# Performance work log

Measured on AMD Instinct MI355X. Metric: run time of the kernel, lower is better.

The kernel has to match this reference:

```python
import jax, jax.numpy as jnp
import numpy as np

DIM = 512
CTX_DIM = 512
NUM_HEADS = 8
DIM_HEAD = 64
INNER = NUM_HEADS * DIM_HEAD  # 512
B, N, CTX_LEN = 4, 2048, 2048


def setup_inputs() -> dict:
    key = jax.random.key(0)
    ks = jax.random.split(key, 6)
    x = jax.random.normal(ks[0], (B, DIM, N), dtype=jnp.float32)
    context = jax.random.normal(ks[1], (B, CTX_DIM, CTX_LEN), dtype=jnp.float32)
    # Linear weights stored as (in, out); bias only on output projection.
    W_q = jax.random.normal(ks[2], (DIM, INNER), dtype=jnp.float32) / np.sqrt(DIM)
    W_kv = jax.random.normal(ks[3], (CTX_DIM, 2 * INNER), dtype=jnp.float32) / np.sqrt(CTX_DIM)
    W_out = jax.random.normal(ks[4], (INNER, DIM), dtype=jnp.float32) / np.sqrt(INNER)
    b_out = jax.random.normal(ks[5], (DIM,), dtype=jnp.float32) * 0.01
    return {"x": x, "context": context, "W_q": W_q, "W_kv": W_kv,
            "W_out": W_out, "b_out": b_out}


def reference(x, context, W_q, W_kv, W_out, b_out):
    scale = DIM_HEAD ** -0.5
    xs = jnp.swapaxes(x, 1, 2)        # (b, n, dim)
    cs = jnp.swapaxes(context, 1, 2)  # (b, ctx_len, ctx_dim)
    b, n, _ = xs.shape
    m = cs.shape[1]
    q = xs @ W_q                       # (b, n, inner)
    kv = cs @ W_kv                     # (b, m, 2*inner)
    k, v = jnp.split(kv, 2, axis=-1)
    # split heads -> (b, h, len, d)
    q = q.reshape(b, n, NUM_HEADS, DIM_HEAD).transpose(0, 2, 1, 3)
    k = k.reshape(b, m, NUM_HEADS, DIM_HEAD).transpose(0, 2, 1, 3)
    v = v.reshape(b, m, NUM_HEADS, DIM_HEAD).transpose(0, 2, 1, 3)
    attn = jnp.einsum('bhqd,bhkd->bhqk', q * scale, k)
    attn = jax.nn.softmax(attn, axis=-1)
    out = jnp.einsum('bhqk,bhkd->bhqd', attn, v)
    out = out.transpose(0, 2, 1, 3).reshape(b, n, INNER)
    out = out @ W_out + b_out          # (b, n, dim); dropout p=0 is identity
    return jnp.swapaxes(out, 1, 2)     # (b, dim, n)
```

## Files before the change

kernel.cpp:

```cpp
#include <hip/hip_runtime.h>
#include <hip/hip_bf16.h>

typedef __attribute__((ext_vector_type(8))) short bf16x8;
typedef __attribute__((ext_vector_type(4))) float f32x4;
typedef __attribute__((ext_vector_type(16))) float f32x16;
typedef __attribute__((ext_vector_type(8))) unsigned short ushort8v;
typedef __attribute__((ext_vector_type(4))) unsigned short ushort4v;

#define MFMA16(a, b, c) __builtin_amdgcn_mfma_f32_16x16x32_bf16((a), (b), (c), 0, 0, 0)
#define MFMA32(a, b, c) __builtin_amdgcn_mfma_f32_32x32x16_bf16((a), (b), (c), 0, 0, 0)

__device__ __forceinline__ unsigned short f2bf(float f) {
  union { float f; unsigned int u; } v; v.f = f;
  unsigned int r = v.u + 0x7FFFu + ((v.u >> 16) & 1u);
  return (unsigned short)(r >> 16);
}

__device__ __forceinline__ unsigned int cvtpk(float a, float b) {
  unsigned int r;
  asm("v_cvt_pk_bf16_f32 %0, %1, %2" : "=v"(r) : "v"(a), "v"(b));
  return r;
}

__global__ __launch_bounds__(256) void transpose_all_kernel(
    const float* __restrict__ x, const float* __restrict__ ctx,
    const float* __restrict__ Wq, const float* __restrict__ Wkv,
    const float* __restrict__ Wo, unsigned short* __restrict__ xt,
    unsigned short* __restrict__ ct, unsigned short* __restrict__ Wqt,
    unsigned short* __restrict__ Wkvt, unsigned short* __restrict__ Wot) {
  __shared__ float tile[64][33];
  int z = blockIdx.z;
  const float* in;
  unsigned short* out;
  int C;
  if (z < 4)      { in = x + (size_t)z * 512 * 2048;         out = xt + (size_t)z * 2048 * 512;        C = 2048; }
  else if (z < 8) { in = ctx + (size_t)(z - 4) * 512 * 2048; out = ct + (size_t)(z - 4) * 2048 * 512;  C = 2048; }
  else if (z == 8) { in = Wq;  out = Wqt;  C = 512; }
  else if (z == 9) { in = Wkv; out = Wkvt; C = 1024; }
  else             { in = Wo;  out = Wot;  C = 512; }
  int c0 = blockIdx.x * 32;
  if (c0 >= C) return;
  int r0 = blockIdx.y * 64;
  int tid = threadIdx.x, cl = tid & 31, rl = tid >> 5;
#pragma unroll
  for (int k = 0; k < 8; ++k)
    tile[rl + 8 * k][cl] = in[(size_t)(r0 + rl + 8 * k) * C + c0 + cl];
  __syncthreads();
  int c = tid >> 3, rc = (tid & 7) * 8;
  ushort8v p;
#pragma unroll
  for (int jj = 0; jj < 8; ++jj) p[jj] = f2bf(tile[rc + jj][c]);
  *(ushort8v*)&out[(size_t)(c0 + c) * 512 + r0 + rc] = p;
}

__device__ __forceinline__ void gemm_acc128(
    const unsigned short* __restrict__ A, const unsigned short* __restrict__ Bt,
    int l0, int o0, f32x4 acc[4][4],
    unsigned short (*As)[80], unsigned short (*Bs)[80]) {
  int tid = threadIdx.x, lane = tid & 63, wave = tid >> 6;
  int wl = wave >> 1, wo = wave & 1, lg = lane >> 4, lr = lane & 15;
  for (int kb = 0; kb < 512; kb += 64) {
    {
      int row = tid >> 1, cc = (tid & 1) * 32;
      const ushort8v* srca = (const ushort8v*)(A + (size_t)(l0 + row) * 512 + kb + cc);
      const ushort8v* srcb = (const ushort8v*)(Bt + (size_t)(o0 + row) * 512 + kb + cc);
#pragma unroll
      for (int i = 0; i < 4; ++i) *(ushort8v*)&As[row][cc + 8 * i] = srca[i];
#pragma unroll
      for (int i = 0; i < 4; ++i) *(ushort8v*)&Bs[row][cc + 8 * i] = srcb[i];
    }
    __syncthreads();
#pragma unroll
    for (int kc = 0; kc < 2; ++kc) {
      bf16x8 af[4], bfr[4];
#pragma unroll
      for (int mf = 0; mf < 4; ++mf)
        af[mf] = *(const bf16x8*)&As[wl * 64 + mf * 16 + lr][kc * 32 + 8 * lg];
#pragma unroll
      for (int nf = 0; nf < 4; ++nf)
        bfr[nf] = *(const bf16x8*)&Bs[wo * 64 + nf * 16 + lr][kc * 32 + 8 * lg];
#pragma unroll
      for (int mf = 0; mf < 4; ++mf)
#pragma unroll
        for (int nf = 0; nf < 4; ++nf)
          acc[mf][nf] = MFMA16(af[mf], bfr[nf], acc[mf][nf]);
    }
    __syncthreads();
  }
}

__global__ __launch_bounds__(256) void gemm_qkv_kernel(
    const unsigned short* __restrict__ xt, const unsigned short* __restrict__ ct,
    const unsigned short* __restrict__ Wqt, const unsigned short* __restrict__ Wkvt,
    unsigned short* __restrict__ Qb, unsigned short* __restrict__ K,
    unsigned short* __restrict__ Vt) {
  __shared__ unsigned short As[128][80];
  __shared__ unsigned short Bs[128][80];
  f32x4 acc[4][4] = {};
  int l0 = blockIdx.x * 128;
  int yy = blockIdx.y;
  const unsigned short* A;
  const unsigned short* Bt;
  int o0;
  if (yy < 4) { A = xt; Bt = Wqt; o0 = yy * 128; }
  else        { A = ct; Bt = Wkvt; o0 = (yy - 4) * 128; }
  gemm_acc128(A, Bt, l0, o0, acc, As, Bs);
  int lane = threadIdx.x & 63, wave = threadIdx.x >> 6;
  int wl = wave >> 1, wo = wave & 1, lg = lane >> 4, lr = lane & 15;
  if (yy < 4) {
    const float qs = 0.18033688011112042f;
#pragma unroll
    for (int mf = 0; mf < 4; ++mf)
#pragma unroll
      for (int nf = 0; nf < 4; ++nf)
#pragma unroll
        for (int r = 0; r < 4; ++r) {
          int row = l0 + wl * 64 + mf * 16 + 4 * lg + r;
          int col = o0 + wo * 64 + nf * 16 + lr;
          Qb[(size_t)row * 512 + col] = f2bf(acc[mf][nf][r] * qs);
        }
  } else if (o0 < 512) {
#pragma unroll
    for (int mf = 0; mf < 4; ++mf)
#pragma unroll
      for (int nf = 0; nf < 4; ++nf)
#pragma unroll
        for (int r = 0; r < 4; ++r) {
          int row = l0 + wl * 64 + mf * 16 + 4 * lg + r;
          int col = o0 + wo * 64 + nf * 16 + lr;
          K[(size_t)row * 512 + col] = f2bf(acc[mf][nf][r]);
        }
  } else {
    int b = l0 >> 11;
#pragma unroll
    for (int mf = 0; mf < 4; ++mf)
#pragma unroll
      for (int nf = 0; nf < 4; ++nf) {
        int m0v = (l0 & 2047) + wl * 64 + mf * 16 + 4 * lg;
        int msw = (m0v & ~12) | ((m0v & 4) << 1) | ((m0v & 8) >> 1);
        int oh = (o0 - 512) + wo * 64 + nf * 16 + lr;
        int h = oh >> 6, d = oh & 63;
        ushort4v pk;
#pragma unroll
        for (int r = 0; r < 4; ++r) pk[r] = f2bf(acc[mf][nf][r]);
        *(ushort4v*)&Vt[(size_t)((b * 8 + h) * 64 + d) * 2048 + msw] = pk;
      }
  }
}

__global__ __launch_bounds__(256) void gemm_out_kernel(
    const unsigned short* __restrict__ A, const unsigned short* __restrict__ Bt,
    float* __restrict__ Out, const float* __restrict__ bias) {
  __shared__ unsigned short As[128][80];
  __shared__ unsigned short Bs[128][80];
  f32x4 acc[4][4] = {};
  int l0 = blockIdx.x * 128, o0 = blockIdx.y * 128;
  gemm_acc128(A, Bt, l0, o0, acc, As, Bs);
  int lane = threadIdx.x & 63, wave = threadIdx.x >> 6;
  int wl = wave >> 1, wo = wave & 1, lg = lane >> 4, lr = lane & 15;
#pragma unroll
  for (int mf = 0; mf < 4; ++mf)
#pragma unroll
    for (int nf = 0; nf < 4; ++nf) {
      int row = l0 + wl * 64 + mf * 16 + 4 * lg;
      int col = o0 + wo * 64 + nf * 16 + lr;
      int b = row >> 11, n = row & 2047;
      float bv = bias[col];
      f32x4 v = acc[mf][nf];
#pragma unroll
      for (int r = 0; r < 4; ++r) v[r] += bv;
      *(f32x4*)&Out[((size_t)(b * 512 + col)) * 2048 + n] = v;
    }
}

__global__ __launch_bounds__(128, 2) void attn_kernel(
    const unsigned short* __restrict__ Qb, const unsigned short* __restrict__ Kb,
    const unsigned short* __restrict__ Vt, unsigned short* __restrict__ Ob) {
  __shared__ unsigned short Ksh[2][4160];
  __shared__ unsigned short Vsh[2][4160];
  int id = blockIdx.x;
  int slot = id & 7, qb = (id >> 3) & 31, hbhi = id >> 8;
  int hb = hbhi * 8 + slot;
  int h = hb & 7, b = hb >> 3;
  int tid = threadIdx.x, w = tid >> 6, lane = tid & 63;
  int l31 = lane & 31, hi = lane >> 5;
  int qrow = b * 2048 + qb * 64 + w * 32 + l31;

  const unsigned short* qp = Qb + (size_t)qrow * 512 + h * 64 + 8 * hi;
  bf16x8 qf[4];
#pragma unroll
  for (int dk = 0; dk < 4; ++dk) qf[dk] = *(const bf16x8*)(qp + 16 * dk);

  int r8 = lane >> 3, gc = (lane & 7) ^ r8;
  const unsigned short* kg =
      Kb + (size_t)(b * 2048 + w * 32 + r8) * 512 + h * 64 + gc * 8;
  const unsigned short* vg =
      Vt + (size_t)((b * 8 + h) * 64 + w * 32 + r8) * 2048 + gc * 8;
  int grp0 = w * 4;

#define STAGE(t, bi)                                                               \
  {                                                                                \
    _Pragma("unroll") for (int j2 = 0; j2 < 4; ++j2) {                             \
      __builtin_amdgcn_global_load_lds(                                            \
          (const __attribute__((address_space(1))) void*)(kg +                     \
              (size_t)((t) * 64 + j2 * 8) * 512),                                  \
          (__attribute__((address_space(3))) void*)(&Ksh[bi][(grp0 + j2) * 520]),  \
          16, 0, 0);                                                               \
      __builtin_amdgcn_global_load_lds(                                            \
          (const __attribute__((address_space(1))) void*)(vg +                     \
              (size_t)(j2 * 8) * 2048 + (t) * 64),                                 \
          (__attribute__((address_space(3))) void*)(&Vsh[bi][(grp0 + j2) * 520]),  \
          16, 0, 0);                                                               \
    }                                                                              \
  }

  STAGE(0, 0);
  STAGE(1, 1);

  int rowoff0 = (l31 >> 3) * 1040 + (l31 & 7) * 128;
  int rowoff1 = rowoff0 + 4 * 1040;
  int swz = (l31 & 7) << 4;

  f32x16 o0 = {}, o1 = {};
  float lsum = 0.0f;

#pragma unroll 1
  for (int t = 0; t < 32; ++t) {
    int bi = t & 1;
    if (t == 31) { asm volatile("s_waitcnt vmcnt(0)" ::: "memory"); }
    else         { asm volatile("s_waitcnt vmcnt(8)" ::: "memory"); }
    __builtin_amdgcn_sched_barrier(0);
    __builtin_amdgcn_s_barrier();
    __builtin_amdgcn_sched_barrier(0);

    const char* kbC = (const char*)&Ksh[bi][0];
    const char* vbC = (const char*)&Vsh[bi][0];
    bf16x8 kfr[8];
#pragma unroll
    for (int dk = 0; dk < 4; ++dk) {
      kfr[dk] = *(const bf16x8*)(kbC + rowoff0 + (((2 * dk + hi) << 4) ^ swz));
      kfr[4 + dk] = *(const bf16x8*)(kbC + rowoff1 + (((2 * dk + hi) << 4) ^ swz));
    }
    bf16x8 vfa[4], vfb[4];
#pragma unroll
    for (int q = 0; q < 4; ++q) {
      vfa[q] = *(const bf16x8*)(vbC + rowoff0 + (((2 * q + hi) << 4) ^ swz));
      vfb[q] = *(const bf16x8*)(vbC + rowoff1 + (((2 * q + hi) << 4) ^ swz));
    }
    asm volatile("s_waitcnt lgkmcnt(0)" ::: "memory");
    __builtin_amdgcn_sched_barrier(0);
    __builtin_amdgcn_s_barrier();
    __builtin_amdgcn_sched_barrier(0);
    if (t < 30) STAGE(t + 2, bi);

    __builtin_amdgcn_s_setprio(1);
    f32x16 sA = {}, sB = {};
#pragma unroll
    for (int dk = 0; dk < 4; ++dk) {
      sA = MFMA32(kfr[dk], qf[dk], sA);
      sB = MFMA32(kfr[4 + dk], qf[dk], sB);
    }
    __builtin_amdgcn_s_setprio(0);

#pragma unroll
    for (int i = 0; i < 16; ++i) {
      sA[i] = __builtin_amdgcn_exp2f(sA[i]);
      sB[i] = __builtin_amdgcn_exp2f(sB[i]);
    }
    float u[8];
#pragma unroll
    for (int i = 0; i < 8; ++i) u[i] = (sA[i] + sA[i + 8]) + (sB[i] + sB[i + 8]);
    lsum += ((u[0] + u[1]) + (u[2] + u[3])) + ((u[4] + u[5]) + (u[6] + u[7]));

    bf16x8 ptA[2], ptB[2];
    {
      union { unsigned int wd[4]; bf16x8 v; } uu;
      uu.wd[0] = cvtpk(sA[0], sA[1]); uu.wd[1] = cvtpk(sA[2], sA[3]);
      uu.wd[2] = cvtpk(sA[4], sA[5]); uu.wd[3] = cvtpk(sA[6], sA[7]);
      ptA[0] = uu.v;
      uu.wd[0] = cvtpk(sA[8], sA[9]); uu.wd[1] = cvtpk(sA[10], sA[11]);
      uu.wd[2] = cvtpk(sA[12], sA[13]); uu.wd[3] = cvtpk(sA[14], sA[15]);
      ptA[1] = uu.v;
      uu.wd[0] = cvtpk(sB[0], sB[1]); uu.wd[1] = cvtpk(sB[2], sB[3]);
      uu.wd[2] = cvtpk(sB[4], sB[5]); uu.wd[3] = cvtpk(sB[6], sB[7]);
      ptB[0] = uu.v;
      uu.wd[0] = cvtpk(sB[8], sB[9]); uu.wd[1] = cvtpk(sB[10], sB[11]);
      uu.wd[2] = cvtpk(sB[12], sB[13]); uu.wd[3] = cvtpk(sB[14], sB[15]);
      ptB[1] = uu.v;
    }

    __builtin_amdgcn_s_setprio(1);
    o0 = MFMA32(vfa[0], ptA[0], o0);
    o0 = MFMA32(vfa[1], ptA[1], o0);
    o1 = MFMA32(vfb[0], ptA[0], o1);
    o1 = MFMA32(vfb[1], ptA[1], o1);
    o0 = MFMA32(vfa[2], ptB[0], o0);
    o0 = MFMA32(vfa[3], ptB[1], o0);
    o1 = MFMA32(vfb[2], ptB[0], o1);
    o1 = MFMA32(vfb[3], ptB[1], o1);
    __builtin_amdgcn_s_setprio(0);
  }
#undef STAGE

  float ltot = lsum + __shfl_xor(lsum, 32, 64);
  float rinv = 1.0f / ltot;
  unsigned short* ob = Ob + (size_t)qrow * 512 + h * 64 + 4 * hi;
#pragma unroll
  for (int i = 0; i < 8; ++i) {
    int dvlo = ((2 * i) & 3) + 8 * ((2 * i) >> 2);
    *(unsigned int*)(ob + dvlo) = cvtpk(o0[2 * i] * rinv, o0[2 * i + 1] * rinv);
    *(unsigned int*)(ob + 32 + dvlo) = cvtpk(o1[2 * i] * rinv, o1[2 * i + 1] * rinv);
  }
}

extern "C" void kernel_launch(void* const* d_in, const int* in_sizes, int n_in,
                              void* d_out, int out_size, void* d_ws, size_t ws_size,
                              hipStream_t stream) {
  const float* x   = (const float*)d_in[0];
  const float* ctx = (const float*)d_in[1];
  const float* Wq  = (const float*)d_in[2];
  const float* Wkv = (const float*)d_in[3];
  const float* Wo  = (const float*)d_in[4];
  const float* bo  = (const float*)d_in[5];
  float* out = (float*)d_out;

  char* ws = (char*)d_ws;
  unsigned short* xt   = (unsigned short*)(ws + 0);
  unsigned short* ct   = (unsigned short*)(ws + 8388608);
  unsigned short* Wqt  = (unsigned short*)(ws + 16777216);
  unsigned short* Wkvt = (unsigned short*)(ws + 17301504);
  unsigned short* Wot  = (unsigned short*)(ws + 18350080);
  unsigned short* Qb   = (unsigned short*)(ws + 18874368);
  unsigned short* Kb   = (unsigned short*)(ws + 27262976);
  unsigned short* Vtb  = (unsigned short*)(ws + 35651584);
  unsigned short* Ob   = (unsigned short*)(ws + 44040192);

  transpose_all_kernel<<<dim3(64, 8, 11), 256, 0, stream>>>(
      x, ctx, Wq, Wkv, Wo, xt, ct, Wqt, Wkvt, Wot);

  gemm_qkv_kernel<<<dim3(64, 12), 256, 0, stream>>>(xt, ct, Wqt, Wkvt, Qb, Kb, Vtb);

  attn_kernel<<<dim3(1024), 128, 0, stream>>>(Qb, Kb, Vtb, Ob);

  gemm_out_kernel<<<dim3(64, 4), 256, 0, stream>>>(Ob, Wot, out, bo);
}
```

Measured before the change: 110.9 us.

## Use direct global-to-LDS loads with XOR-swizzled layout in projection GEMMs

Replaces the register-staged global-to-shared copies in the shared GEMM tile routine with global_load_lds direct-to-LDS transfers. The shared-memory layout becomes an XOR-swizzled 8-row block layout so MFMA fragment reads avoid bank conflicts. Separately, bf16 conversion switches from manual integer rounding to the packed hardware v_cvt_pk_bf16_f32 instruction in the transpose and epilogues. This removes VGPR staging and conversion ALU work, at the cost of more complex addressing. The main attention kernel is unaffected, so the overall effect is bounded by the GEMM share of the total time.

```diff
diff --git a/kernel.cpp b/kernel.cpp
--- a/kernel.cpp
+++ b/kernel.cpp
@@ -10,16 +10,13 @@
 #define MFMA16(a, b, c) __builtin_amdgcn_mfma_f32_16x16x32_bf16((a), (b), (c), 0, 0, 0)
 #define MFMA32(a, b, c) __builtin_amdgcn_mfma_f32_32x32x16_bf16((a), (b), (c), 0, 0, 0)
 
-__device__ __forceinline__ unsigned short f2bf(float f) {
-  union { float f; unsigned int u; } v; v.f = f;
-  unsigned int r = v.u + 0x7FFFu + ((v.u >> 16) & 1u);
-  return (unsigned short)(r >> 16);
-}
-
 __device__ __forceinline__ unsigned int cvtpk(float a, float b) {
   unsigned int r;
   asm("v_cvt_pk_bf16_f32 %0, %1, %2" : "=v"(r) : "v"(a), "v"(b));
   return r;
+}
+__device__ __forceinline__ unsigned short f2bf(float f) {
+  return (unsigned short)cvtpk(f, f);
 }
 
 __global__ __launch_bounds__(256) void transpose_all_kernel(
@@ -47,27 +44,43 @@
     tile[rl + 8 * k][cl] = in[(size_t)(r0 + rl + 8 * k) * C + c0 + cl];
   __syncthreads();
   int c = tid >> 3, rc = (tid & 7) * 8;
-  ushort8v p;
-#pragma unroll
-  for (int jj = 0; jj < 8; ++jj) p[jj] = f2bf(tile[rc + jj][c]);
-  *(ushort8v*)&out[(size_t)(c0 + c) * 512 + r0 + rc] = p;
+  union { unsigned int wd[4]; ushort8v v; } p;
+#pragma unroll
+  for (int jj = 0; jj < 4; ++jj)
+    p.wd[jj] = cvtpk(tile[rc + 2 * jj][c], tile[rc + 2 * jj + 1][c]);
+  *(ushort8v*)&out[(size_t)(c0 + c) * 512 + r0 + rc] = p.v;
 }
 
 __device__ __forceinline__ void gemm_acc128(
     const unsigned short* __restrict__ A, const unsigned short* __restrict__ Bt,
     int l0, int o0, f32x4 acc[4][4],
-    unsigned short (*As)[80], unsigned short (*Bs)[80]) {
-  int tid = threadIdx.x, lane = tid & 63, wave = tid >> 6;
-  int wl = wave >> 1, wo = wave & 1, lg = lane >> 4, lr = lane & 15;
+    unsigned short* As, unsigned short* Bs) {
+  int tid = threadIdx.x, lane = tid & 63, wv = tid >> 6;
+  int wl = wv >> 1, wo = wv & 1, lg = lane >> 4, lr = lane & 15;
+  int r8 = lane >> 3, gc = (lane & 7) ^ r8;
+  const unsigned short* ga = A + (size_t)(l0 + wv * 32 + r8) * 512 + gc * 8;
+  const unsigned short* gb = Bt + (size_t)(o0 + wv * 32 + r8) * 512 + gc * 8;
+  int rowbA[4], rswA[4], rowbB[4], rswB[4];
+#pragma unroll
+  for (int f = 0; f < 4; ++f) {
+    int r = wl * 64 + f * 16 + lr;
+    rowbA[f] = (r >> 3) * 1040 + (r & 7) * 128;
+    rswA[f] = (r & 7) << 4;
+    int rb = wo * 64 + f * 16 + lr;
+    rowbB[f] = (rb >> 3) * 1040 + (rb & 7) * 128;
+    rswB[f] = (rb & 7) << 4;
+  }
+  const char* aC = (const char*)As;
+  const char* bC = (const char*)Bs;
   for (int kb = 0; kb < 512; kb += 64) {
-    {
-      int row = tid >> 1, cc = (tid & 1) * 32;
-      const ushort8v* srca = (const ushort8v*)(A + (size_t)(l0 + row) * 512 + kb + cc);
-      const ushort8v* srcb = (const ushort8v*)(Bt + (size_t)(o0 + row) * 512 + kb + cc);
-#pragma unroll
-      for (int i = 0; i < 4; ++i) *(ushort8v*)&As[row][cc + 8 * i] = srca[i];
-#pragma unroll
-      for (int i = 0; i < 4; ++i) *(ushort8v*)&Bs[row][cc + 8 * i] = srcb[i];
+#pragma unroll
+    for (int j = 0; j < 4; ++j) {
+      __builtin_amdgcn_global_load_lds(
+          (const __attribute__((address_space(1))) void*)(ga + (size_t)(j * 8) * 512 + kb),
+          (__attribute__((address_space(3))) void*)(As + (wv * 4 + j) * 520), 16, 0, 0);
+      __builtin_amdgcn_global_load_lds(
+          (const __attribute__((address_space(1))) void*)(gb + (size_t)(j * 8) * 512 + kb),
+          (__attribute__((address_space(3))) void*)(Bs + (wv * 4 + j) * 520), 16, 0, 0);
     }
     __syncthreads();
 #pragma unroll
@@ -75,10 +88,10 @@
       bf16x8 af[4], bfr[4];
 #pragma unroll
       for (int mf = 0; mf < 4; ++mf)
-        af[mf] = *(const bf16x8*)&As[wl * 64 + mf * 16 + lr][kc * 32 + 8 * lg];
+        af[mf] = *(const bf16x8*)(aC + rowbA[mf] + (((4 * kc + lg) << 4) ^ rswA[mf]));
 #pragma unroll
       for (int nf = 0; nf < 4; ++nf)
-        bfr[nf] = *(const bf16x8*)&Bs[wo * 64 + nf * 16 + lr][kc * 32 + 8 * lg];
+        bfr[nf] = *(const bf16x8*)(bC + rowbB[nf] + (((4 * kc + lg) << 4) ^ rswB[nf]));
 #pragma unroll
       for (int mf = 0; mf < 4; ++mf)
 #pragma unroll
@@ -94,8 +107,8 @@
     const unsigned short* __restrict__ Wqt, const unsigned short* __restrict__ Wkvt,
     unsigned short* __restrict__ Qb, unsigned short* __restrict__ K,
     unsigned short* __restrict__ Vt) {
-  __shared__ unsigned short As[128][80];
-  __shared__ unsigned short Bs[128][80];
+  __shared__ unsigned short As[8320];
+  __shared__ unsigned short Bs[8320];
   f32x4 acc[4][4] = {};
   int l0 = blockIdx.x * 128;
   int yy = blockIdx.y;
@@ -151,8 +164,8 @@
 __global__ __launch_bounds__(256) void gemm_out_kernel(
     const unsigned short* __restrict__ A, const unsigned short* __restrict__ Bt,
     float* __restrict__ Out, const float* __restrict__ bias) {
-  __shared__ unsigned short As[128][80];
-  __shared__ unsigned short Bs[128][80];
+  __shared__ unsigned short As[8320];
+  __shared__ unsigned short Bs[8320];
   f32x4 acc[4][4] = {};
   int l0 = blockIdx.x * 128, o0 = blockIdx.y * 128;
   gemm_acc128(A, Bt, l0, o0, acc, As, Bs);
```

Result: faster. 96.91 us (-12.7%).
